# Optimization experiments

Hardware: AMD Instinct MI355X
Metric: run time of the kernel (lower is better)

The kernel has to match this reference:

```python
import jax, jax.numpy as jnp
import numpy as np

B, N_IN, N_MID, N_OUT = 262144, 64, 128, 32


def setup_inputs() -> dict:
    key = jax.random.key(0)
    kx, k1, kb1, k2, kb2 = jax.random.split(key, 5)
    v1 = 1.0 / np.sqrt(N_IN)   # per-synapse init range sqrt(1/len(dendrites))
    v2 = 1.0 / np.sqrt(N_MID)
    return {
        "x": jax.random.normal(kx, (B, N_IN), dtype=jnp.float32),
        "W1": jax.random.uniform(k1, (N_IN, N_MID), minval=-v1, maxval=v1, dtype=jnp.float32),
        "b1": jnp.zeros((N_MID,), dtype=jnp.float32),  # obtain_float_parameter inits biases to 0.0
        "W2": jax.random.uniform(k2, (N_MID, N_OUT), minval=-v2, maxval=v2, dtype=jnp.float32),
        "b2": jnp.zeros((N_OUT,), dtype=jnp.float32),
    }


def reference(x, W1, b1, W2, b2):
    # RegularNeuron: sum_i k_ij * x_i + b_j, then ReLU
    h = jax.nn.relu(x @ W1 + b1)          # [B, N_MID]
    # Output DestinationNeuron: sum_j k_jo * h_j + b_o, no activation
    y = h @ W2 + b2                        # [B, N_OUT]
    return y
```

## Files before the change

### kernel.cpp

```cpp
#include <hip/hip_runtime.h>
#include <hip/hip_bf16.h>

#define B_ROWS 262144
#define N_TILES (B_ROWS / 16)

typedef short short8 __attribute__((ext_vector_type(8)));
typedef float f32x4 __attribute__((ext_vector_type(4)));

__device__ inline short f2bf(float f) {
    __hip_bfloat16 h = __float2bfloat16(f);
    return __builtin_bit_cast(short, h);
}

__global__ __launch_bounds__(256, 2) void livenet_mlp(
    const float* __restrict__ x, const float* __restrict__ W1,
    const float* __restrict__ b1, const float* __restrict__ W2,
    const float* __restrict__ b2, float* __restrict__ y) {
    __shared__ short hbuf[4 * 2048];

    const int tid  = threadIdx.x;
    const int wid  = tid >> 6;
    const int lane = tid & 63;
    const int g    = lane >> 4;
    const int q    = lane & 15;
    short* hb = hbuf + wid * 2048;

    short8 w1f[2][8];
#pragma unroll
    for (int ks = 0; ks < 2; ++ks)
#pragma unroll
        for (int n = 0; n < 8; ++n) {
            short8 v;
#pragma unroll
            for (int j = 0; j < 8; ++j)
                v[j] = f2bf(W1[(ks * 32 + g * 8 + j) * 128 + n * 16 + q]);
            w1f[ks][n] = v;
        }
    short8 w2f[4][2];
#pragma unroll
    for (int ks = 0; ks < 4; ++ks)
#pragma unroll
        for (int n = 0; n < 2; ++n) {
            short8 v;
#pragma unroll
            for (int j = 0; j < 8; ++j)
                v[j] = f2bf(W2[(ks * 32 + g * 8 + j) * 32 + n * 16 + q]);
            w2f[ks][n] = v;
        }
    float b1v[8], b2v[2];
#pragma unroll
    for (int n = 0; n < 8; ++n) b1v[n] = b1[n * 16 + q];
#pragma unroll
    for (int n = 0; n < 2; ++n) b2v[n] = b2[n * 16 + q];

    const int gwave    = blockIdx.x * 4 + wid;
    const int n_gwaves = gridDim.x * 4;

    f32x4 cur[4], nxt[4];
    {
        const f32x4* p = (const f32x4*)(x + (size_t)(gwave * 16 + q) * 64 + g * 8);
        cur[0] = p[0];
        cur[1] = p[1];
        cur[2] = p[8];
        cur[3] = p[9];
    }

    for (int tile = gwave; tile < N_TILES; tile += n_gwaves) {
        const int tn = tile + n_gwaves;
        if (tn < N_TILES) {
            const f32x4* p = (const f32x4*)(x + (size_t)(tn * 16 + q) * 64 + g * 8);
            nxt[0] = p[0];
            nxt[1] = p[1];
            nxt[2] = p[8];
            nxt[3] = p[9];
        }

        const int row0 = tile * 16;

        short8 a[2];
#pragma unroll
        for (int ks = 0; ks < 2; ++ks) {
            f32x4 lo = cur[ks * 2 + 0];
            f32x4 hi = cur[ks * 2 + 1];
            short8 v;
            v[0] = f2bf(lo[0]); v[1] = f2bf(lo[1]); v[2] = f2bf(lo[2]); v[3] = f2bf(lo[3]);
            v[4] = f2bf(hi[0]); v[5] = f2bf(hi[1]); v[6] = f2bf(hi[2]); v[7] = f2bf(hi[3]);
            a[ks] = v;
        }

        f32x4 acc1[8];
#pragma unroll
        for (int n = 0; n < 8; ++n)
            acc1[n] = (f32x4){b1v[n], b1v[n], b1v[n], b1v[n]};
#pragma unroll
        for (int ks = 0; ks < 2; ++ks)
#pragma unroll
            for (int n = 0; n < 8; ++n)
                acc1[n] = __builtin_amdgcn_mfma_f32_16x16x32_bf16(a[ks], w1f[ks][n], acc1[n], 0, 0, 0);

#pragma unroll
        for (int n = 0; n < 8; ++n) {
#pragma unroll
            for (int r = 0; r < 4; ++r) {
                const int rr = g * 4 + r;
                const int c  = n * 16 + q;
                float hv = acc1[n][r];
                hv = hv > 0.0f ? hv : 0.0f;
                const int off = (rr * 128 + c) ^ ((rr & 7) << 3);
                hb[off] = f2bf(hv);
            }
        }

        short8 ha[4];
#pragma unroll
        for (int ks = 0; ks < 4; ++ks) {
            const int off = (q * 128 + ks * 32 + g * 8) ^ ((q & 7) << 3);
            ha[ks] = *(const short8*)&hb[off];
        }

        f32x4 acc2[2];
#pragma unroll
        for (int n = 0; n < 2; ++n)
            acc2[n] = (f32x4){b2v[n], b2v[n], b2v[n], b2v[n]};
#pragma unroll
        for (int ks = 0; ks < 4; ++ks)
#pragma unroll
            for (int n = 0; n < 2; ++n)
                acc2[n] = __builtin_amdgcn_mfma_f32_16x16x32_bf16(ha[ks], w2f[ks][n], acc2[n], 0, 0, 0);

#pragma unroll
        for (int n = 0; n < 2; ++n)
#pragma unroll
            for (int r = 0; r < 4; ++r)
                __builtin_nontemporal_store(
                    acc2[n][r], y + (size_t)(row0 + g * 4 + r) * 32 + n * 16 + q);

        cur[0] = nxt[0]; cur[1] = nxt[1]; cur[2] = nxt[2]; cur[3] = nxt[3];
    }
}

extern "C" void kernel_launch(void* const* d_in, const int* in_sizes, int n_in,
                              void* d_out, int out_size, void* d_ws, size_t ws_size,
                              hipStream_t stream) {
    const float* x  = (const float*)d_in[0];
    const float* W1 = (const float*)d_in[1];
    const float* b1 = (const float*)d_in[2];
    const float* W2 = (const float*)d_in[3];
    const float* b2 = (const float*)d_in[4];
    float* y = (float*)d_out;

    const int blocks = 512;
    livenet_mlp<<<blocks, 256, 0, stream>>>(x, W1, b1, W2, b2, y);
}
```

Measured before the change: 24.73 us.

## Swap MFMA operands to get transposed outputs for vectorized LDS and global stores

Swaps the A/B operands of both MFMAs so each lane holds four consecutive output columns of one row instead of four rows of one column. This lets the hidden activations be packed and written to LDS as 8-byte stores with a new swizzle, and lets the final output be written as one 16-byte nontemporal store per fragment instead of four scalar stores. Bias is loaded as vectors directly into the accumulator init. The aim is fewer LDS and global store instructions, at the cost of a more intricate swizzle that must stay correct and bank-conflict free.

Result: faster. 24.03 us (-2.9%).

```diff
diff --git a/kernel.cpp b/kernel.cpp
--- a/kernel.cpp
+++ b/kernel.cpp
@@ -11,12 +11,17 @@
     __hip_bfloat16 h = __float2bfloat16(f);
     return __builtin_bit_cast(short, h);
 }
+__device__ inline unsigned pk2(float a, float b) {
+    unsigned lo = (unsigned short)f2bf(a);
+    unsigned hi = (unsigned short)f2bf(b);
+    return lo | (hi << 16);
+}
 
 __global__ __launch_bounds__(256, 2) void livenet_mlp(
     const float* __restrict__ x, const float* __restrict__ W1,
     const float* __restrict__ b1, const float* __restrict__ W2,
     const float* __restrict__ b2, float* __restrict__ y) {
-    __shared__ short hbuf[4 * 2048];
+    __shared__ __align__(16) short hbuf[4 * 2048];
 
     const int tid  = threadIdx.x;
     const int wid  = tid >> 6;
@@ -24,6 +29,7 @@
     const int g    = lane >> 4;
     const int q    = lane & 15;
     short* hb = hbuf + wid * 2048;
+    const int key = 2 * (q & 7);
 
     short8 w1f[2][8];
 #pragma unroll
@@ -47,11 +53,13 @@
                 v[j] = f2bf(W2[(ks * 32 + g * 8 + j) * 32 + n * 16 + q]);
             w2f[ks][n] = v;
         }
-    float b1v[8], b2v[2];
+    f32x4 binit1[8], binit2[2];
 #pragma unroll
-    for (int n = 0; n < 8; ++n) b1v[n] = b1[n * 16 + q];
+    for (int n = 0; n < 8; ++n)
+        binit1[n] = *(const f32x4*)(b1 + n * 16 + 4 * g);
 #pragma unroll
-    for (int n = 0; n < 2; ++n) b2v[n] = b2[n * 16 + q];
+    for (int n = 0; n < 2; ++n)
+        binit2[n] = *(const f32x4*)(b2 + n * 16 + 4 * g);
 
     const int gwave    = blockIdx.x * 4 + wid;
     const int n_gwaves = gridDim.x * 4;
@@ -59,20 +67,14 @@
     f32x4 cur[4], nxt[4];
     {
         const f32x4* p = (const f32x4*)(x + (size_t)(gwave * 16 + q) * 64 + g * 8);
-        cur[0] = p[0];
-        cur[1] = p[1];
-        cur[2] = p[8];
-        cur[3] = p[9];
+        cur[0] = p[0]; cur[1] = p[1]; cur[2] = p[8]; cur[3] = p[9];
     }
 
     for (int tile = gwave; tile < N_TILES; tile += n_gwaves) {
         const int tn = tile + n_gwaves;
         if (tn < N_TILES) {
             const f32x4* p = (const f32x4*)(x + (size_t)(tn * 16 + q) * 64 + g * 8);
-            nxt[0] = p[0];
-            nxt[1] = p[1];
-            nxt[2] = p[8];
-            nxt[3] = p[9];
+            nxt[0] = p[0]; nxt[1] = p[1]; nxt[2] = p[8]; nxt[3] = p[9];
         }
 
         const int row0 = tile * 16;
@@ -90,50 +92,44 @@
 
         f32x4 acc1[8];
 #pragma unroll
-        for (int n = 0; n < 8; ++n)
-            acc1[n] = (f32x4){b1v[n], b1v[n], b1v[n], b1v[n]};
-#pragma unroll
-        for (int ks = 0; ks < 2; ++ks)
-#pragma unroll
-            for (int n = 0; n < 8; ++n)
-                acc1[n] = __builtin_amdgcn_mfma_f32_16x16x32_bf16(a[ks], w1f[ks][n], acc1[n], 0, 0, 0);
+        for (int n = 0; n < 8; ++n) {
+            acc1[n] = __builtin_amdgcn_mfma_f32_16x16x32_bf16(w1f[0][n], a[0], binit1[n], 0, 0, 0);
+            acc1[n] = __builtin_amdgcn_mfma_f32_16x16x32_bf16(w1f[1][n], a[1], acc1[n], 0, 0, 0);
+        }
 
 #pragma unroll
         for (int n = 0; n < 8; ++n) {
-#pragma unroll
-            for (int r = 0; r < 4; ++r) {
-                const int rr = g * 4 + r;
-                const int c  = n * 16 + q;
-                float hv = acc1[n][r];
-                hv = hv > 0.0f ? hv : 0.0f;
-                const int off = (rr * 128 + c) ^ ((rr & 7) << 3);
-                hb[off] = f2bf(hv);
-            }
+            float h0 = fmaxf(acc1[n][0], 0.0f);
+            float h1 = fmaxf(acc1[n][1], 0.0f);
+            float h2 = fmaxf(acc1[n][2], 0.0f);
+            float h3 = fmaxf(acc1[n][3], 0.0f);
+            uint2 w;
+            w.x = pk2(h0, h1);
+            w.y = pk2(h2, h3);
+            const int cbp = (4 * n + g) ^ key;
+            ((uint2*)hb)[q * 32 + cbp] = w;
         }
 
         short8 ha[4];
 #pragma unroll
         for (int ks = 0; ks < 4; ++ks) {
-            const int off = (q * 128 + ks * 32 + g * 8) ^ ((q & 7) << 3);
-            ha[ks] = *(const short8*)&hb[off];
+            const int cbr = (8 * ks + 2 * g) ^ key;
+            ha[ks] = *(const short8*)&hb[q * 128 + 4 * cbr];
         }
 
         f32x4 acc2[2];
 #pragma unroll
-        for (int n = 0; n < 2; ++n)
-            acc2[n] = (f32x4){b2v[n], b2v[n], b2v[n], b2v[n]};
+        for (int n = 0; n < 2; ++n) {
+            acc2[n] = __builtin_amdgcn_mfma_f32_16x16x32_bf16(w2f[0][n], ha[0], binit2[n], 0, 0, 0);
 #pragma unroll
-        for (int ks = 0; ks < 4; ++ks)
-#pragma unroll
-            for (int n = 0; n < 2; ++n)
-                acc2[n] = __builtin_amdgcn_mfma_f32_16x16x32_bf16(ha[ks], w2f[ks][n], acc2[n], 0, 0, 0);
+            for (int ks = 1; ks < 4; ++ks)
+                acc2[n] = __builtin_amdgcn_mfma_f32_16x16x32_bf16(w2f[ks][n], ha[ks], acc2[n], 0, 0, 0);
+        }
 
 #pragma unroll
         for (int n = 0; n < 2; ++n)
-#pragma unroll
-            for (int r = 0; r < 4; ++r)
-                __builtin_nontemporal_store(
-                    acc2[n][r], y + (size_t)(row0 + g * 4 + r) * 32 + n * 16 + q);
+            __builtin_nontemporal_store(
+                acc2[n], (f32x4*)(y + (size_t)(row0 + q) * 32 + n * 16 + 4 * g));
 
         cur[0] = nxt[0]; cur[1] = nxt[1]; cur[2] = nxt[2]; cur[3] = nxt[3];
     }
```
